# Optimization experiments

Hardware: AMD Instinct MI355X
Metric: run time of the kernel (lower is better)

The kernel has to match this reference:

```python
import jax, jax.numpy as jnp
import numpy as np

FACTOR = 1.0   # module's self.factor
EPS = 1e-6     # rmsnorm eps


def setup_inputs() -> dict:
    key = jax.random.key(0)
    k0, k1, k2, k3 = jax.random.split(key, 4)
    B, S = 4, 2048
    D_IN = D_STATE = D_OUT = 2048
    N_HEADS = 32
    HD = D_STATE // N_HEADS  # 64
    x = jax.random.normal(k0, (B, S, D_IN), jnp.float32)
    w_in = jax.random.normal(k1, (D_STATE, D_IN), jnp.float32) * 0.02
    b_in = jnp.zeros((D_STATE,), jnp.float32)
    state_weight = jax.random.normal(k2, (N_HEADS, HD, HD), jnp.float32) * 0.02
    norm_weight = jnp.ones((D_STATE,), jnp.float32)
    w_out = jax.random.normal(k3, (D_OUT, D_STATE), jnp.float32) * (0.02 / np.sqrt(2 * 24))
    return dict(x=x, w_in=w_in, b_in=b_in, state_weight=state_weight,
                norm_weight=norm_weight, w_out=w_out)


def _rnn_scan(xt, W):
    # xt: (B, S, N, H); W: (N, H, H)
    B, S, N, H = xt.shape

    def step(s, x_t):
        # s: (B, N, H) ; per-head linear recurrence with tanh nonlinearity
        s = jnp.tanh(jnp.einsum('bnh,nhk->bnk', s, W) + x_t)
        return s, s

    s0 = jnp.zeros((B, N, H), xt.dtype)
    _, states = jax.lax.scan(step, s0, jnp.swapaxes(xt, 0, 1))  # (S, B, N, H)
    return jnp.swapaxes(states, 0, 1)  # (B, S, N, H)


def reference(x, w_in, b_in, state_weight, norm_weight, w_out):
    B, S, _ = x.shape
    N, H, _ = state_weight.shape
    h = x @ w_in.T + b_in                      # input_projection: (B,S,state)
    h = h.reshape(B, S, N, H) * FACTOR
    W = state_weight * FACTOR
    states = _rnn_scan(h, W)                   # (B,S,N,H)
    y = states.reshape(B, S, N * H)
    # rmsnorm
    y = y * jax.lax.rsqrt(jnp.mean(y * y, axis=-1, keepdims=True) + EPS) * norm_weight
    return y @ w_out.T                         # output_projection (no bias)
```

## Files before the change

kernel.cpp:

```cpp
#include <hip/hip_runtime.h>
#include <hip/hip_bf16.h>
#include <cstdint>


typedef short bf16x8 __attribute__((ext_vector_type(8)));
typedef float f32x4 __attribute__((ext_vector_type(4)));
typedef float f32x2 __attribute__((ext_vector_type(2)));

#define GLD16(gp, lp)                                                          \
  __builtin_amdgcn_global_load_lds(                                            \
      (const __attribute__((address_space(1))) void*)(gp),                     \
      (__attribute__((address_space(3))) void*)(lp), 16, 0, 0)

__global__ __launch_bounds__(256) void cvt_f32_bf16(
    const float* __restrict__ in, __hip_bfloat16* __restrict__ out, int n4) {
  int i = blockIdx.x * 256 + threadIdx.x;
  if (i >= n4) return;
  float4 v = ((const float4*)in)[i];
  __hip_bfloat16 a = __float2bfloat16(v.x);
  __hip_bfloat16 b = __float2bfloat16(v.y);
  __hip_bfloat16 c = __float2bfloat16(v.z);
  __hip_bfloat16 d = __float2bfloat16(v.w);
  ushort4 p;
  p.x = *(unsigned short*)&a; p.y = *(unsigned short*)&b;
  p.z = *(unsigned short*)&c; p.w = *(unsigned short*)&d;
  ((ushort4*)out)[i] = p;
}

__global__ __launch_bounds__(256) void gemm_nt(
    const __hip_bfloat16* __restrict__ A, const __hip_bfloat16* __restrict__ B,
    const float* __restrict__ bias, float* __restrict__ C,
    int M, int N, int K) {
  __shared__ __hip_bfloat16 As[128 * 32];
  __shared__ __hip_bfloat16 Bs[128 * 32];
  const int tid  = threadIdx.x;
  const int lane = tid & 63;
  const int wave = tid >> 6;
  const int wm = wave >> 1, wn = wave & 1;
  const long bm = (long)blockIdx.y * 128;
  const long bn = (long)blockIdx.x * 128;

  const int c0 = tid, c1 = tid + 256;
  const int r0 = c0 >> 2, k0 = (c0 & 3) * 8;
  const int r1 = c1 >> 2, k1 = (c1 & 3) * 8;
  __hip_bfloat16* lA0 = &As[(wave * 64) * 8];
  __hip_bfloat16* lA1 = &As[(256 + wave * 64) * 8];
  __hip_bfloat16* lB0 = &Bs[(wave * 64) * 8];
  __hip_bfloat16* lB1 = &Bs[(256 + wave * 64) * 8];
  const __hip_bfloat16* gA0 = A + (bm + r0) * (long)K + k0;
  const __hip_bfloat16* gA1 = A + (bm + r1) * (long)K + k1;
  const __hip_bfloat16* gB0 = B + (bn + r0) * (long)K + k0;
  const __hip_bfloat16* gB1 = B + (bn + r1) * (long)K + k1;

  const int fr = lane & 15;
  const int fk = (lane >> 4) * 8;

  f32x4 acc[4][4];
#pragma unroll
  for (int i = 0; i < 4; i++)
#pragma unroll
    for (int j = 0; j < 4; j++) acc[i][j] = {0.f, 0.f, 0.f, 0.f};

  for (int kt = 0; kt < K; kt += 32) {
    __syncthreads();
    GLD16(gA0 + kt, lA0);
    GLD16(gA1 + kt, lA1);
    GLD16(gB0 + kt, lB0);
    GLD16(gB1 + kt, lB1);
    __syncthreads();
    bf16x8 af[4], bfr[4];
#pragma unroll
    for (int t = 0; t < 4; t++)
      af[t] = *(const bf16x8*)&As[(wm * 64 + t * 16 + fr) * 32 + fk];
#pragma unroll
    for (int t = 0; t < 4; t++)
      bfr[t] = *(const bf16x8*)&Bs[(wn * 64 + t * 16 + fr) * 32 + fk];
#pragma unroll
    for (int i = 0; i < 4; i++)
#pragma unroll
      for (int j = 0; j < 4; j++)
        acc[i][j] = __builtin_amdgcn_mfma_f32_16x16x32_bf16(
            af[i], bfr[j], acc[i][j], 0, 0, 0);
  }

  const int cr = (lane >> 4) * 4;
  const int cc = lane & 15;
#pragma unroll
  for (int j = 0; j < 4; j++) {
    const long n = bn + wn * 64 + j * 16 + cc;
    const float bv = bias ? bias[n] : 0.0f;
#pragma unroll
    for (int i = 0; i < 4; i++) {
      const long m = bm + wm * 64 + i * 16 + cr;
#pragma unroll
      for (int r = 0; r < 4; r++)
        C[(m + r) * (long)N + n] = acc[i][j][r] + bv;
    }
  }
}

__device__ __forceinline__ void pk_fma(f32x2& d, f32x2 a, f32x2 b) {
  asm("v_pk_fma_f32 %0, %1, %2, %0" : "+v"(d) : "v"(a), "v"(b));
}

__device__ __forceinline__ float tanh_fast(float z) {
  float e = __expf(2.0f * z);
  return 1.0f - 2.0f * __builtin_amdgcn_rcpf(e + 1.0f);
}

__global__ __launch_bounds__(64) void scan_kernel(
    const float* __restrict__ Wst, float* __restrict__ h) {
  const int b = blockIdx.x >> 5;
  const int n = blockIdx.x & 31;
  const int lane = threadIdx.x;
  const float* Wn = Wst + n * 4096;
  f32x2 w2[32];
#pragma unroll
  for (int j = 0; j < 32; j++) {
    f32x2 t;
    t.x = Wn[(2 * j) * 64 + lane];
    t.y = Wn[(2 * j + 1) * 64 + lane];
    w2[j] = t;
  }

  __shared__ float s_lds[64];

  float4 sv[16];
#pragma unroll
  for (int i = 0; i < 16; i++) sv[i] = make_float4(0.f, 0.f, 0.f, 0.f);

  float* hp = h + ((size_t)b * 2048) * 2048 + n * 64 + lane;
  float xcur[8], xnxt[8];
#pragma unroll
  for (int i = 0; i < 8; i++) xcur[i] = hp[(size_t)i * 2048];

  for (int t0 = 0; t0 < 2048; t0 += 8) {
    if (t0 + 8 < 2048) {
#pragma unroll
      for (int i = 0; i < 8; i++)
        xnxt[i] = hp[(size_t)(t0 + 8 + i) * 2048];
    }
#pragma unroll
    for (int i = 0; i < 8; i++) {
      f32x2 acc[4];
      acc[0].x = xcur[i]; acc[0].y = 0.f;
      acc[1] = acc[2] = acc[3] = f32x2{0.f, 0.f};
#pragma unroll
      for (int q = 0; q < 16; q++) {
        f32x2 lo; lo.x = sv[q].x; lo.y = sv[q].y;
        f32x2 hi; hi.x = sv[q].z; hi.y = sv[q].w;
        pk_fma(acc[(2 * q) & 3], lo, w2[2 * q]);
        pk_fma(acc[(2 * q + 1) & 3], hi, w2[2 * q + 1]);
      }
      f32x2 s01 = acc[0] + acc[1];
      f32x2 s23 = acc[2] + acc[3];
      f32x2 st = s01 + s23;
      float sn = tanh_fast(st.x + st.y);
      s_lds[lane] = sn;
#pragma unroll
      for (int q = 0; q < 16; q++) sv[q] = ((const float4*)s_lds)[q];
      hp[(size_t)(t0 + i) * 2048] = sn;
    }
#pragma unroll
    for (int i = 0; i < 8; i++) xcur[i] = xnxt[i];
  }
}

__global__ __launch_bounds__(256) void rmsnorm_to_bf16(
    const float* __restrict__ Y, const float* __restrict__ g,
    __hip_bfloat16* __restrict__ O) {
  const long row = blockIdx.x;
  const float* yr = Y + row * 2048;
  const int tid = threadIdx.x;
  float4 v0 = ((const float4*)yr)[tid * 2];
  float4 v1 = ((const float4*)yr)[tid * 2 + 1];
  float ss = v0.x * v0.x + v0.y * v0.y + v0.z * v0.z + v0.w * v0.w +
             v1.x * v1.x + v1.y * v1.y + v1.z * v1.z + v1.w * v1.w;
#pragma unroll
  for (int off = 32; off > 0; off >>= 1) ss += __shfl_down(ss, off);
  __shared__ float red[4];
  if ((tid & 63) == 0) red[tid >> 6] = ss;
  __syncthreads();
  float inv = rsqrtf((red[0] + red[1] + red[2] + red[3]) * (1.0f / 2048.0f)
                     + 1e-6f);
  float4 g0 = ((const float4*)(g + tid * 8))[0];
  float4 g1 = ((const float4*)(g + tid * 8))[1];
  float ov[8] = {v0.x * inv * g0.x, v0.y * inv * g0.y,
                 v0.z * inv * g0.z, v0.w * inv * g0.w,
                 v1.x * inv * g1.x, v1.y * inv * g1.y,
                 v1.z * inv * g1.z, v1.w * inv * g1.w};
  ushort4 p0, p1;
  __hip_bfloat16 t;
  t = __float2bfloat16(ov[0]); p0.x = *(unsigned short*)&t;
  t = __float2bfloat16(ov[1]); p0.y = *(unsigned short*)&t;
  t = __float2bfloat16(ov[2]); p0.z = *(unsigned short*)&t;
  t = __float2bfloat16(ov[3]); p0.w = *(unsigned short*)&t;
  t = __float2bfloat16(ov[4]); p1.x = *(unsigned short*)&t;
  t = __float2bfloat16(ov[5]); p1.y = *(unsigned short*)&t;
  t = __float2bfloat16(ov[6]); p1.z = *(unsigned short*)&t;
  t = __float2bfloat16(ov[7]); p1.w = *(unsigned short*)&t;
  ushort4* op = (ushort4*)(O + row * 2048 + tid * 8);
  op[0] = p0;
  op[1] = p1;
}

extern "C" void kernel_launch(void* const* d_in, const int* in_sizes, int n_in,
                              void* d_out, int out_size, void* d_ws,
                              size_t ws_size, hipStream_t stream) {
  const float* x     = (const float*)d_in[0];
  const float* w_in  = (const float*)d_in[1];
  const float* b_in  = (const float*)d_in[2];
  const float* w_st  = (const float*)d_in[3];
  const float* nw    = (const float*)d_in[4];
  const float* w_out = (const float*)d_in[5];
  float* out = (float*)d_out;

  char* ws = (char*)d_ws;
  __hip_bfloat16* x_bf  = (__hip_bfloat16*)(ws);
  __hip_bfloat16* wi_bf = (__hip_bfloat16*)(ws + 33554432);
  __hip_bfloat16* wo_bf = (__hip_bfloat16*)(ws + 41943040);
  float* h              = (float*)(ws + 50331648);

  cvt_f32_bf16<<<16384, 256, 0, stream>>>(x, x_bf, 4194304);
  cvt_f32_bf16<<<4096, 256, 0, stream>>>(w_in, wi_bf, 1048576);
  cvt_f32_bf16<<<4096, 256, 0, stream>>>(w_out, wo_bf, 1048576);

  gemm_nt<<<dim3(16, 64), 256, 0, stream>>>(x_bf, wi_bf, b_in, h,
                                            8192, 2048, 2048);
  scan_kernel<<<128, 64, 0, stream>>>(w_st, h);
  rmsnorm_to_bf16<<<8192, 256, 0, stream>>>(h, nw, x_bf);
  gemm_nt<<<dim3(16, 64), 256, 0, stream>>>(x_bf, wo_bf, nullptr, out,
                                            8192, 2048, 2048);
}
```

Measured before the change: 795.3 us.

## Interleave two batch recurrences per wave in the RNN scan kernel

Each scan block now processes two batch elements for the same head, interleaving their independent recurrence steps within a single wave and sharing the loaded state weights. This halves the number of blocks but aims to hide the latency of the serial FMA/tanh/LDS chain with instruction-level parallelism. The cost is roughly doubled live register state and fewer active CUs, with a risk of spills.

```diff
diff --git a/kernel.cpp b/kernel.cpp
--- a/kernel.cpp
+++ b/kernel.cpp
@@ -110,8 +110,8 @@
 
 __global__ __launch_bounds__(64) void scan_kernel(
     const float* __restrict__ Wst, float* __restrict__ h) {
-  const int b = blockIdx.x >> 5;
-  const int n = blockIdx.x & 31;
+  const int n  = blockIdx.x >> 1;
+  const int bp = blockIdx.x & 1;
   const int lane = threadIdx.x;
   const float* Wn = Wst + n * 4096;
   f32x2 w2[32];
@@ -123,46 +123,78 @@
     w2[j] = t;
   }
 
-  __shared__ float s_lds[64];
-
-  float4 sv[16];
-#pragma unroll
-  for (int i = 0; i < 16; i++) sv[i] = make_float4(0.f, 0.f, 0.f, 0.f);
-
-  float* hp = h + ((size_t)b * 2048) * 2048 + n * 64 + lane;
-  float xcur[8], xnxt[8];
-#pragma unroll
-  for (int i = 0; i < 8; i++) xcur[i] = hp[(size_t)i * 2048];
+  __shared__ float sA[64];
+  __shared__ float sB[64];
+
+  float4 svA[16], svB[16];
+#pragma unroll
+  for (int i = 0; i < 16; i++) {
+    svA[i] = make_float4(0.f, 0.f, 0.f, 0.f);
+    svB[i] = make_float4(0.f, 0.f, 0.f, 0.f);
+  }
+
+  float* hpA = h + ((size_t)(2 * bp) * 2048) * 2048 + n * 64 + lane;
+  float* hpB = h + ((size_t)(2 * bp + 1) * 2048) * 2048 + n * 64 + lane;
+  float xAc[8], xAn[8], xBc[8], xBn[8];
+#pragma unroll
+  for (int i = 0; i < 8; i++) {
+    xAc[i] = hpA[(size_t)i * 2048];
+    xBc[i] = hpB[(size_t)i * 2048];
+  }
 
   for (int t0 = 0; t0 < 2048; t0 += 8) {
     if (t0 + 8 < 2048) {
 #pragma unroll
-      for (int i = 0; i < 8; i++)
-        xnxt[i] = hp[(size_t)(t0 + 8 + i) * 2048];
+      for (int i = 0; i < 8; i++) {
+        xAn[i] = hpA[(size_t)(t0 + 8 + i) * 2048];
+        xBn[i] = hpB[(size_t)(t0 + 8 + i) * 2048];
+      }
     }
 #pragma unroll
     for (int i = 0; i < 8; i++) {
-      f32x2 acc[4];
-      acc[0].x = xcur[i]; acc[0].y = 0.f;
-      acc[1] = acc[2] = acc[3] = f32x2{0.f, 0.f};
-#pragma unroll
-      for (int q = 0; q < 16; q++) {
-        f32x2 lo; lo.x = sv[q].x; lo.y = sv[q].y;
-        f32x2 hi; hi.x = sv[q].z; hi.y = sv[q].w;
-        pk_fma(acc[(2 * q) & 3], lo, w2[2 * q]);
-        pk_fma(acc[(2 * q + 1) & 3], hi, w2[2 * q + 1]);
+      {
+        f32x2 acc[4];
+        acc[0].x = xAc[i]; acc[0].y = 0.f;
+        acc[1] = acc[2] = acc[3] = f32x2{0.f, 0.f};
+#pragma unroll
+        for (int q = 0; q < 16; q++) {
+          f32x2 lo; lo.x = svA[q].x; lo.y = svA[q].y;
+          f32x2 hi; hi.x = svA[q].z; hi.y = svA[q].w;
+          pk_fma(acc[(2 * q) & 3], lo, w2[2 * q]);
+          pk_fma(acc[(2 * q + 1) & 3], hi, w2[2 * q + 1]);
+        }
+        f32x2 s01 = acc[0] + acc[1];
+        f32x2 s23 = acc[2] + acc[3];
+        f32x2 st = s01 + s23;
+        float sn = tanh_fast(st.x + st.y);
+        sA[lane] = sn;
+#pragma unroll
+        for (int q = 0; q < 16; q++) svA[q] = ((const float4*)sA)[q];
+        hpA[(size_t)(t0 + i) * 2048] = sn;
       }
-      f32x2 s01 = acc[0] + acc[1];
-      f32x2 s23 = acc[2] + acc[3];
-      f32x2 st = s01 + s23;
-      float sn = tanh_fast(st.x + st.y);
-      s_lds[lane] = sn;
-#pragma unroll
-      for (int q = 0; q < 16; q++) sv[q] = ((const float4*)s_lds)[q];
-      hp[(size_t)(t0 + i) * 2048] = sn;
+      {
+        f32x2 acc[4];
+        acc[0].x = xBc[i]; acc[0].y = 0.f;
+        acc[1] = acc[2] = acc[3] = f32x2{0.f, 0.f};
+#pragma unroll
+        for (int q = 0; q < 16; q++) {
+          f32x2 lo; lo.x = svB[q].x; lo.y = svB[q].y;
+          f32x2 hi; hi.x = svB[q].z; hi.y = svB[q].w;
+          pk_fma(acc[(2 * q) & 3], lo, w2[2 * q]);
+          pk_fma(acc[(2 * q + 1) & 3], hi, w2[2 * q + 1]);
+        }
+        f32x2 s01 = acc[0] + acc[1];
+        f32x2 s23 = acc[2] + acc[3];
+        f32x2 st = s01 + s23;
+        float sn = tanh_fast(st.x + st.y);
+        sB[lane] = sn;
+#pragma unroll
+        for (int q = 0; q < 16; q++) svB[q] = ((const float4*)sB)[q];
+        hpB[(size_t)(t0 + i) * 2048] = sn;
+      }
     }
 #pragma unroll
-    for (int i = 0; i < 8; i++) xcur[i] = xnxt[i];
+    for (int i = 0; i < 8; i++) { xAc[i] = xAn[i]; xBc[i] = xBn[i]; }
   }
 }
 
@@ -227,7 +259,7 @@
 
   gemm_nt<<<dim3(16, 64), 256, 0, stream>>>(x_bf, wi_bf, b_in, h,
                                             8192, 2048, 2048);
-  scan_kernel<<<128, 64, 0, stream>>>(w_st, h);
+  scan_kernel<<<64, 64, 0, stream>>>(w_st, h);
   rmsnorm_to_bf16<<<8192, 256, 0, stream>>>(h, nw, x_bf);
   gemm_nt<<<dim3(16, 64), 256, 0, stream>>>(x_bf, wo_bf, nullptr, out,
                                             8192, 2048, 2048);
```

After: 1.071 ms. 34.7% more time.
